# Kernel optimization log

Measured on AMD Instinct MI355X. Metric: run time of the kernel, lower is better.

The kernel has to match this reference:

```python
import jax, jax.numpy as jnp
import numpy as np

ISQRT2 = 0.7071067811865476  # 1/sqrt(2), haar analysis/synthesis coefficient
LEVELS = 13                  # pywt.dwt_max_level(8192, 'haar') = log2(8192)
J = 4                        # recursion_limit
BN_EPS = 1e-5


def haar_wavedec(x, levels):
    """Full-depth haar DWT (mode='zero' is exact for power-of-2 length).
    x: [..., N]. Returns bank [cA_L, cD_L, cD_{L-1}, ..., cD_1] (pywt order).
    Vectorized over batch AND channel dims at once (the per-channel python
    loop in the torch module computes identical math per channel)."""
    a = x
    details = []
    for _ in range(levels):
        even, odd = a[..., ::2], a[..., 1::2]
        details.append((even - odd) * ISQRT2)
        a = (even + odd) * ISQRT2
    return [a] + details[::-1]


def haar_waverec(bank):
    """Inverse of haar_wavedec; bank in pywt order [cA, cD_coarse..cD_fine]."""
    a = bank[0]
    for d in bank[1:]:
        up = jnp.stack([a + d, a - d], axis=-1) * ISQRT2  # interleave even/odd
        a = up.reshape(a.shape[:-1] + (a.shape[-1] * 2,))
    return a


def batch_norm_train(y, g, b):
    # BatchNorm1d training mode: stats over (batch, length) per channel, biased var
    mean = jnp.mean(y, axis=(0, 2), keepdims=True)
    var = jnp.var(y, axis=(0, 2), keepdims=True)
    return (y - mean) * jax.lax.rsqrt(var + BN_EPS) * g[None, :, None] + b[None, :, None]


def reference(x, gamma, beta):
    # x: [B, C, N]; gamma, beta: [J, C]
    bank = haar_wavedec(x, LEVELS)  # computed once, reused for all masks
    zeros_bank = [jnp.zeros_like(c) for c in bank]

    # masked_inputs[j]: IWT keeping only band j (pool_inputs=False -> full bank)
    masked_inputs = []
    for j in range(J):
        mb = [bank[i] if i == j else zeros_bank[i] for i in range(len(bank))]
        masked_inputs.append(haar_waverec(mb))

    # masked_targets[j]: IWT keeping bands 0..j (pool_targets=False)
    masked_targets = []
    for j in range(J):
        mb = [bank[i] if i <= j else zeros_bank[i] for i in range(len(bank))]
        masked_targets.append(haar_waverec(mb))

    # per-level BatchNorm on inputs only
    masked_inputs = [batch_norm_train(masked_inputs[j], gamma[j], beta[j]) for j in range(J)]

    # stack for a single output tensor: [2, J, B, C, N]
    return jnp.stack([jnp.stack(masked_inputs), jnp.stack(masked_targets)])


def setup_inputs() -> dict:
    key = jax.random.key(0)
    x = jax.random.normal(key, (64, 16, 8192), dtype=jnp.float32)
    gamma = jnp.ones((J, 16), dtype=jnp.float32)
    beta = jnp.zeros((J, 16), dtype=jnp.float32)
    return {"x": x, "gamma": gamma, "beta": beta}
```

## Files before the change

### kernel.cpp

```cpp
#include <hip/hip_runtime.h>


#define NROWS 1024
#define ROWLEN 8192
#define STATS_STRIDE 16

typedef float f32x4 __attribute__((ext_vector_type(4)));

__global__ __launch_bounds__(256) void row_stats_kernel(const float* __restrict__ x,
                                                        float* __restrict__ stats) {
    int row = blockIdx.x;
    const f32x4* xr = reinterpret_cast<const f32x4*>(x) + (size_t)row * (ROWLEN / 4);
    int t = threadIdx.x;
    float s[8];
#pragma unroll
    for (int k = 0; k < 8; ++k) {
        f32x4 v = __builtin_nontemporal_load(&xr[t + 256 * k]);
        s[k] = (v.x + v.y) + (v.z + v.w);
    }
    __shared__ float red[8][4];
    __shared__ float m3s[8];
    int lane = t & 63, wave = t >> 6;
#pragma unroll
    for (int k = 0; k < 8; ++k) {
        float v = s[k];
#pragma unroll
        for (int off = 32; off; off >>= 1) v += __shfl_down(v, off, 64);
        if (lane == 0) red[k][wave] = v;
    }
    __syncthreads();
    if (t < 8) m3s[t] = (red[t][0] + red[t][1] + red[t][2] + red[t][3]) * (1.0f / 1024.0f);
    __syncthreads();
    if (t == 0) {
        float* o = stats + (size_t)row * STATS_STRIDE;
        float m2[4], m1[2];
#pragma unroll
        for (int k = 0; k < 4; ++k) m2[k] = 0.5f * (m3s[2 * k] + m3s[2 * k + 1]);
        m1[0] = 0.5f * (m2[0] + m2[1]);
        m1[1] = 0.5f * (m2[2] + m2[3]);
        float m0 = 0.5f * (m1[0] + m1[1]);
        o[0] = m0;
        o[1] = m1[0]; o[2] = m1[1];
        o[3] = m2[0]; o[4] = m2[1]; o[5] = m2[2]; o[6] = m2[3];
#pragma unroll
        for (int k = 0; k < 8; ++k) o[7 + k] = m3s[k];
    }
}

__global__ __launch_bounds__(64) void bn_stats_kernel(const float* __restrict__ stats,
                                                      const float* __restrict__ gamma,
                                                      const float* __restrict__ beta,
                                                      float* __restrict__ bn ) {
    int j = blockIdx.x >> 4;
    int c = blockIdx.x & 15;
    int b = threadIdx.x;
    const float* s = stats + (size_t)((b << 4) + c) * STATS_STRIDE;
    float sum = 0.f, sum2 = 0.f;
    float B = (float)(ROWLEN >> j);
    if (j == 0) {
        float d = s[0];
        sum = d; sum2 = d * d;
    } else {
        int base = (1 << j) - 1;
        int pbase = (1 << (j - 1)) - 1;
        int nb = 1 << j;
        for (int k = 0; k < nb; ++k) {
            float d = s[base + k] - s[pbase + (k >> 1)];
            sum += d; sum2 += d * d;
        }
    }
    sum *= B; sum2 *= B;
#pragma unroll
    for (int off = 32; off; off >>= 1) {
        sum  += __shfl_down(sum, off, 64);
        sum2 += __shfl_down(sum2, off, 64);
    }
    if (b == 0) {
        const float N = 64.0f * 8192.0f;
        float mean = sum / N;
        float var = sum2 / N - mean * mean;
        float inv = rsqrtf(var + 1e-5f);
        float scale = gamma[(j << 4) + c] * inv;
        float shift = beta[(j << 4) + c] - mean * scale;
        bn[((j << 4) + c) * 2 + 0] = scale;
        bn[((j << 4) + c) * 2 + 1] = shift;
    }
}

__global__ __launch_bounds__(256) void write_out_kernel(const float* __restrict__ stats,
                                                        const float* __restrict__ bn,
                                                        f32x4* __restrict__ out) {
    unsigned blk = blockIdx.x;
    unsigned c = blk & 15u;
    unsigned b = (blk >> 4) & 63u;
    unsigned j = (blk >> 10) & 3u;
    unsigned part = blk >> 12;
    unsigned nb = 1u << j;
    unsigned t = threadIdx.x;
    __shared__ float sv[8];
    if (t < nb) {
        const float* s = stats + (size_t)((b << 4) + c) * STATS_STRIDE;
        float mj = s[nb - 1u + t];
        float v;
        if (part) {
            v = mj;
        } else {
            float d = mj;
            if (j > 0) d -= s[(nb >> 1) - 1u + (t >> 1)];
            unsigned jc = (j << 4) + c;
            v = d * bn[jc * 2] + bn[jc * 2 + 1];
        }
        sv[t] = v;
    }
    __syncthreads();
    f32x4* orow = out + (size_t)blk * 2048;
    unsigned sh = 3u - j;
#pragma unroll
    for (unsigned i = 0; i < 8; ++i) {
        float v = sv[i >> sh];
        f32x4 q = {v, v, v, v};
        __builtin_nontemporal_store(q, &orow[t + (i << 8)]);
    }
}

extern "C" void kernel_launch(void* const* d_in, const int* in_sizes, int n_in,
                              void* d_out, int out_size, void* d_ws, size_t ws_size,
                              hipStream_t stream) {
    const float* x     = (const float*)d_in[0];
    const float* gamma = (const float*)d_in[1];
    const float* beta  = (const float*)d_in[2];
    float* out = (float*)d_out;

    float* stats = (float*)d_ws;
    float* bn    = stats + (size_t)NROWS * STATS_STRIDE;

    row_stats_kernel<<<NROWS, 256, 0, stream>>>(x, stats);
    bn_stats_kernel<<<64, 64, 0, stream>>>(stats, gamma, beta, bn);
    write_out_kernel<<<8192, 256, 0, stream>>>(stats, bn, (f32x4*)out);
}
```

Before: 62.23 us.

## Fuse target writes into stats kernel and BN stats into input-write kernel

The masked-target outputs now come straight from the row-stats kernel, so the kernel that reads x also writes half of the output. The separate BN statistics kernel is removed: each block of the new inputs kernel recomputes the per-(level, channel) scale and shift from the row stats, then writes four rows. This cuts the launch count from three to two and overlaps target writes with the input read, at the cost of redundant BN reductions across blocks and longer per-block write loops.

```diff
diff --git a/kernel.cpp b/kernel.cpp
--- a/kernel.cpp
+++ b/kernel.cpp
@@ -1,17 +1,16 @@
 #include <hip/hip_runtime.h>
 
 
-#define NROWS 1024
-#define ROWLEN 8192
 #define STATS_STRIDE 16
 
 typedef float f32x4 __attribute__((ext_vector_type(4)));
 
-__global__ __launch_bounds__(256) void row_stats_kernel(const float* __restrict__ x,
-                                                        float* __restrict__ stats) {
+__global__ __launch_bounds__(256) void stats_targets_kernel(const float* __restrict__ x,
+                                                            float* __restrict__ stats,
+                                                            f32x4* __restrict__ out) {
     int row = blockIdx.x;
-    const f32x4* xr = reinterpret_cast<const f32x4*>(x) + (size_t)row * (ROWLEN / 4);
     int t = threadIdx.x;
+    const f32x4* xr = reinterpret_cast<const f32x4*>(x) + (size_t)row * 2048;
     float s[8];
 #pragma unroll
     for (int k = 0; k < 8; ++k) {
@@ -19,7 +18,7 @@
         s[k] = (v.x + v.y) + (v.z + v.w);
     }
     __shared__ float red[8][4];
-    __shared__ float m3s[8];
+    __shared__ float sb[16];
     int lane = t & 63, wave = t >> 6;
 #pragma unroll
     for (int k = 0; k < 8; ++k) {
@@ -29,97 +28,90 @@
         if (lane == 0) red[k][wave] = v;
     }
     __syncthreads();
-    if (t < 8) m3s[t] = (red[t][0] + red[t][1] + red[t][2] + red[t][3]) * (1.0f / 1024.0f);
+    if (t < 8) sb[7 + t] = (red[t][0] + red[t][1] + red[t][2] + red[t][3]) * (1.0f / 1024.0f);
     __syncthreads();
     if (t == 0) {
-        float* o = stats + (size_t)row * STATS_STRIDE;
         float m2[4], m1[2];
 #pragma unroll
-        for (int k = 0; k < 4; ++k) m2[k] = 0.5f * (m3s[2 * k] + m3s[2 * k + 1]);
+        for (int k = 0; k < 4; ++k) m2[k] = 0.5f * (sb[7 + 2 * k] + sb[7 + 2 * k + 1]);
         m1[0] = 0.5f * (m2[0] + m2[1]);
         m1[1] = 0.5f * (m2[2] + m2[3]);
-        float m0 = 0.5f * (m1[0] + m1[1]);
-        o[0] = m0;
-        o[1] = m1[0]; o[2] = m1[1];
-        o[3] = m2[0]; o[4] = m2[1]; o[5] = m2[2]; o[6] = m2[3];
+        sb[0] = 0.5f * (m1[0] + m1[1]);
+        sb[1] = m1[0]; sb[2] = m1[1];
+        sb[3] = m2[0]; sb[4] = m2[1]; sb[5] = m2[2]; sb[6] = m2[3];
+    }
+    __syncthreads();
+    if (t < 15) stats[(size_t)row * STATS_STRIDE + t] = sb[t];
 #pragma unroll
-        for (int k = 0; k < 8; ++k) o[7 + k] = m3s[k];
+    for (int j = 0; j < 4; ++j) {
+        f32x4* orow = out + ((size_t)(4 + j) * 1024 + row) * 2048;
+        int sh = 3 - j;
+#pragma unroll
+        for (int i = 0; i < 8; ++i) {
+            float v = sb[(1 << j) - 1 + (i >> sh)];
+            f32x4 q = {v, v, v, v};
+            __builtin_nontemporal_store(q, &orow[t + (i << 8)]);
+        }
     }
 }
 
-__global__ __launch_bounds__(64) void bn_stats_kernel(const float* __restrict__ stats,
-                                                      const float* __restrict__ gamma,
-                                                      const float* __restrict__ beta,
-                                                      float* __restrict__ bn ) {
-    int j = blockIdx.x >> 4;
-    int c = blockIdx.x & 15;
-    int b = threadIdx.x;
-    const float* s = stats + (size_t)((b << 4) + c) * STATS_STRIDE;
-    float sum = 0.f, sum2 = 0.f;
-    float B = (float)(ROWLEN >> j);
-    if (j == 0) {
-        float d = s[0];
-        sum = d; sum2 = d * d;
-    } else {
-        int base = (1 << j) - 1;
-        int pbase = (1 << (j - 1)) - 1;
-        int nb = 1 << j;
-        for (int k = 0; k < nb; ++k) {
-            float d = s[base + k] - s[pbase + (k >> 1)];
-            sum += d; sum2 += d * d;
+__global__ __launch_bounds__(256) void inputs_kernel(const float* __restrict__ stats,
+                                                     const float* __restrict__ gamma,
+                                                     const float* __restrict__ beta,
+                                                     f32x4* __restrict__ out) {
+    int blk = blockIdx.x;
+    int j = blk >> 8;
+    int c = (blk >> 4) & 15;
+    int bg = blk & 15;
+    int t = threadIdx.x;
+    __shared__ float ss[2];
+    if (t < 64) {
+        const float* s = stats + (size_t)((t << 4) + c) * STATS_STRIDE;
+        float sum = 0.f, sum2 = 0.f;
+        float B = (float)(8192 >> j);
+        if (j == 0) {
+            float d = s[0];
+            sum = d; sum2 = d * d;
+        } else {
+            int base = (1 << j) - 1, pb = (1 << (j - 1)) - 1;
+            for (int k = 0; k < (1 << j); ++k) {
+                float d = s[base + k] - s[pb + (k >> 1)];
+                sum += d; sum2 += d * d;
+            }
+        }
+        sum *= B; sum2 *= B;
+#pragma unroll
+        for (int off = 32; off; off >>= 1) {
+            sum  += __shfl_down(sum, off, 64);
+            sum2 += __shfl_down(sum2, off, 64);
+        }
+        if (t == 0) {
+            const float N = 64.0f * 8192.0f;
+            float mean = sum / N;
+            float var = sum2 / N - mean * mean;
+            float inv = rsqrtf(var + 1e-5f);
+            float sc = gamma[(j << 4) + c] * inv;
+            ss[0] = sc;
+            ss[1] = beta[(j << 4) + c] - mean * sc;
         }
     }
-    sum *= B; sum2 *= B;
+    __syncthreads();
+    float sc = ss[0], sh0 = ss[1];
+    int shr = 3 - j;
 #pragma unroll
-    for (int off = 32; off; off >>= 1) {
-        sum  += __shfl_down(sum, off, 64);
-        sum2 += __shfl_down(sum2, off, 64);
-    }
-    if (b == 0) {
-        const float N = 64.0f * 8192.0f;
-        float mean = sum / N;
-        float var = sum2 / N - mean * mean;
-        float inv = rsqrtf(var + 1e-5f);
-        float scale = gamma[(j << 4) + c] * inv;
-        float shift = beta[(j << 4) + c] - mean * scale;
-        bn[((j << 4) + c) * 2 + 0] = scale;
-        bn[((j << 4) + c) * 2 + 1] = shift;
-    }
-}
-
-__global__ __launch_bounds__(256) void write_out_kernel(const float* __restrict__ stats,
-                                                        const float* __restrict__ bn,
-                                                        f32x4* __restrict__ out) {
-    unsigned blk = blockIdx.x;
-    unsigned c = blk & 15u;
-    unsigned b = (blk >> 4) & 63u;
-    unsigned j = (blk >> 10) & 3u;
-    unsigned part = blk >> 12;
-    unsigned nb = 1u << j;
-    unsigned t = threadIdx.x;
-    __shared__ float sv[8];
-    if (t < nb) {
-        const float* s = stats + (size_t)((b << 4) + c) * STATS_STRIDE;
-        float mj = s[nb - 1u + t];
-        float v;
-        if (part) {
-            v = mj;
-        } else {
-            float d = mj;
-            if (j > 0) d -= s[(nb >> 1) - 1u + (t >> 1)];
-            unsigned jc = (j << 4) + c;
-            v = d * bn[jc * 2] + bn[jc * 2 + 1];
+    for (int bb = 0; bb < 4; ++bb) {
+        int row = (((bg << 2) + bb) << 4) + c;
+        const float* s = stats + (size_t)row * STATS_STRIDE;
+        f32x4* orow = out + ((size_t)j * 1024 + row) * 2048;
+#pragma unroll
+        for (int i = 0; i < 8; ++i) {
+            int run = i >> shr;
+            float mj = s[(1 << j) - 1 + run];
+            float d = (j == 0) ? mj : mj - s[(1 << (j - 1)) - 1 + (run >> 1)];
+            float v = d * sc + sh0;
+            f32x4 q = {v, v, v, v};
+            __builtin_nontemporal_store(q, &orow[t + (i << 8)]);
         }
-        sv[t] = v;
-    }
-    __syncthreads();
-    f32x4* orow = out + (size_t)blk * 2048;
-    unsigned sh = 3u - j;
-#pragma unroll
-    for (unsigned i = 0; i < 8; ++i) {
-        float v = sv[i >> sh];
-        f32x4 q = {v, v, v, v};
-        __builtin_nontemporal_store(q, &orow[t + (i << 8)]);
     }
 }
 
@@ -129,12 +121,9 @@
     const float* x     = (const float*)d_in[0];
     const float* gamma = (const float*)d_in[1];
     const float* beta  = (const float*)d_in[2];
-    float* out = (float*)d_out;
+    f32x4* out = (f32x4*)d_out;
+    float* stats = (float*)d_ws;
 
-    float* stats = (float*)d_ws;
-    float* bn    = stats + (size_t)NROWS * STATS_STRIDE;
-
-    row_stats_kernel<<<NROWS, 256, 0, stream>>>(x, stats);
-    bn_stats_kernel<<<64, 64, 0, stream>>>(stats, gamma, beta, bn);
-    write_out_kernel<<<8192, 256, 0, stream>>>(stats, bn, (f32x4*)out);
+    stats_targets_kernel<<<1024, 256, 0, stream>>>(x, stats, out);
+    inputs_kernel<<<1024, 256, 0, stream>>>(stats, gamma, beta, out);
 }
```

Result: faster. 58.05 us (-6.7%).
